# Performance work log

Hardware: AMD Instinct MI355X
Metric: run time of the kernel (lower is better)

The kernel has to match this reference:

```python
import jax, jax.numpy as jnp
import numpy as np

B, N, HID, HEADS = 4, 512, 64, 4
D = HID // HEADS          # head_dim = 16
E_DIM = 1
SCALE = 1.0 / np.sqrt(D)
LN_EPS = 1e-5
NEG = -1e9


def _linear_init(k, fan_in, fan_out):
    lim = 1.0 / np.sqrt(fan_in)
    kw, kb = jax.random.split(k)
    W = jax.random.uniform(kw, (fan_in, fan_out), jnp.float32, -lim, lim)
    b = jax.random.uniform(kb, (fan_out,), jnp.float32, -lim, lim)
    return W, b


def setup_inputs() -> dict:
    key = jax.random.key(0)
    ks = jax.random.split(key, 8)
    W1_w, W1_b = _linear_init(ks[3], HID, HID)
    W2_w, W2_b = _linear_init(ks[4], HID, HID)
    W3_w, W3_b = _linear_init(ks[5], HID, HID)
    W4_w, W4_b = _linear_init(ks[6], HID, HID)
    W5_w, W5_b = _linear_init(ks[7], E_DIM, HID)
    return {
        "x": jax.random.normal(ks[0], (B, N, HID), jnp.float32),
        "adj": jax.random.randint(ks[1], (B, N, N), 0, 2, jnp.int32),
        "edge_features": jax.random.normal(ks[2], (B, N, N, E_DIM), jnp.float32),
        "W1_w": W1_w, "W1_b": W1_b,
        "W2_w": W2_w, "W2_b": W2_b,
        "W3_w": W3_w, "W3_b": W3_b,
        "W4_w": W4_w, "W4_b": W4_b,
        "W5_w": W5_w, "W5_b": W5_b,
        "ln_g": jnp.ones((HID,), jnp.float32),
        "ln_b": jnp.zeros((HID,), jnp.float32),
    }


def _layer_norm(y, g, b):
    m = jnp.mean(y, axis=-1, keepdims=True)
    v = jnp.mean(jnp.square(y - m), axis=-1, keepdims=True)
    return (y - m) * jax.lax.rsqrt(v + LN_EPS) * g + b


def reference(x, adj, edge_features, W1_w, W1_b, W2_w, W2_b, W3_w, W3_b,
              W4_w, W4_b, W5_w, W5_b, ln_g, ln_b):
    b, n, h = x.shape
    self_t = x @ W1_w + W1_b                               # [B,N,HID]
    Q = (x @ W3_w + W3_b).reshape(b, n, HEADS, D)          # [B,N,H,D]
    K = (x @ W4_w + W4_b).reshape(b, n, HEADS, D)          # [B,N,H,D]
    # edge contribution: W5 e_ij -> [B,N,N,H,D] (the big intermediate)
    Ec = (edge_features @ W5_w + W5_b).reshape(b, n, n, HEADS, D)
    # (Q_i . (K_j + E_ij)) split into node-pair GEMM + edge broadcast term
    scores = (jnp.einsum('bihd,bjhd->bhij', Q, K)
              + jnp.einsum('bihd,bijhd->bhij', Q, Ec)) * SCALE  # [B,H,N,N]
    scores = jnp.where(adj[:, None, :, :] == 0, NEG, scores)
    attn = jax.nn.softmax(scores, axis=-1)                 # dropout = identity (eval)
    V = (x @ W2_w + W2_b).reshape(b, n, HEADS, D)          # [B,N,H,D]
    msg = jnp.einsum('bhij,bjhd->bihd', attn, V).reshape(b, n, h)
    return _layer_norm(x + self_t + msg, ln_g, ln_b)
```

## Files before the change

### kernel.cpp

```cpp
#include <hip/hip_runtime.h>

#define B 4
#define N 512
#define HID 64
#define HEADS 4
#define DH 16
#define SCALE 0.25f
#define NEG (-1e9f)
#define LN_EPS 1e-5f

constexpr int ROWS = B * N;
constexpr size_t OFF_ST  = 0;
constexpr size_t OFF_Q   = (size_t)ROWS * HID;
constexpr size_t OFF_K   = 2 * OFF_Q;
constexpr size_t OFF_V   = 3 * OFF_Q;
constexpr size_t OFF_MSG = 4 * OFF_Q;

__global__ __launch_bounds__(256) void proj_kernel(
    const float* __restrict__ x,
    const float* __restrict__ W1w, const float* __restrict__ W1b,
    const float* __restrict__ W2w, const float* __restrict__ W2b,
    const float* __restrict__ W3w, const float* __restrict__ W3b,
    const float* __restrict__ W4w, const float* __restrict__ W4b,
    float* __restrict__ ws)
{
  __shared__ float xsT[64 * 8];
  const int t = threadIdx.x;
  const int rows0 = blockIdx.x * 8;

  if (t < 128) {
    const float4 v = *(const float4*)&x[(size_t)rows0 * HID + t * 4];
    const int r = t >> 4;
    const int k0 = (t & 15) * 4;
    xsT[(k0 + 0) * 8 + r] = v.x;
    xsT[(k0 + 1) * 8 + r] = v.y;
    xsT[(k0 + 2) * 8 + r] = v.z;
    xsT[(k0 + 3) * 8 + r] = v.w;
  }
  __syncthreads();

  const int m = t >> 6;
  const int c = t & 63;
  const float* Ww; const float* Wb; size_t off;
  if      (m == 0) { Ww = W1w; Wb = W1b; off = OFF_ST; }
  else if (m == 1) { Ww = W3w; Wb = W3b; off = OFF_Q;  }
  else if (m == 2) { Ww = W4w; Wb = W4b; off = OFF_K;  }
  else             { Ww = W2w; Wb = W2b; off = OFF_V;  }

  float acc[8];
#pragma unroll
  for (int r = 0; r < 8; ++r) acc[r] = 0.f;

#pragma unroll 16
  for (int k = 0; k < 64; ++k) {
    const float w = Ww[(k << 6) + c];
    const float* xr = &xsT[k * 8];
    const float4 a0 = *(const float4*)(xr);
    const float4 a1 = *(const float4*)(xr + 4);
    acc[0] = fmaf(a0.x, w, acc[0]); acc[1] = fmaf(a0.y, w, acc[1]);
    acc[2] = fmaf(a0.z, w, acc[2]); acc[3] = fmaf(a0.w, w, acc[3]);
    acc[4] = fmaf(a1.x, w, acc[4]); acc[5] = fmaf(a1.y, w, acc[5]);
    acc[6] = fmaf(a1.z, w, acc[6]); acc[7] = fmaf(a1.w, w, acc[7]);
  }

  const float bias = Wb[c];
  const size_t base = off + (size_t)rows0 * HID + c;
#pragma unroll
  for (int r = 0; r < 8; ++r)
    ws[base + (size_t)r * HID] = acc[r] + bias;
}

__global__ __launch_bounds__(256, 2) void attn_kernel(
    const int*   __restrict__ adj,
    const float* __restrict__ efeat,
    const float* __restrict__ W5w, const float* __restrict__ W5b,
    float* __restrict__ ws)
{
  __shared__ float Ksh[N * 20];
  __shared__ float Vsh[N * 20];

  const int it = blockIdx.x, h = blockIdx.y, b = blockIdx.z;
  const int t = threadIdx.x;
  const int g  = t & 15;
  const int il = t >> 4;
  const int i  = it * 16 + il;

  const float* Qb = ws + OFF_Q;
  const float* Kb = ws + OFF_K;
  const float* Vb = ws + OFF_V;
  float* msg = ws + OFF_MSG;

  {
    const int jj = t >> 2;
    const int dq = (t & 3) << 2;
#pragma unroll
    for (int p = 0; p < 8; ++p) {
      const int j = jj + (p << 6);
      const size_t gb = ((size_t)(b * N + j)) * HID + h * DH + dq;
      *(float4*)&Ksh[j * 20 + dq] = *(const float4*)&Kb[gb];
      *(float4*)&Vsh[j * 20 + dq] = *(const float4*)&Vb[gb];
    }
  }

  const float* qrow = Qb + ((size_t)(b * N + i)) * HID + h * DH;
  const float4 q0 = *(const float4*)(qrow);
  const float4 q1 = *(const float4*)(qrow + 4);
  const float4 q2 = *(const float4*)(qrow + 8);
  const float4 q3 = *(const float4*)(qrow + 12);
  const float4 w50 = *(const float4*)&W5w[h * DH];
  const float4 w51 = *(const float4*)&W5w[h * DH + 4];
  const float4 w52 = *(const float4*)&W5w[h * DH + 8];
  const float4 w53 = *(const float4*)&W5w[h * DH + 12];
  const float4 b50 = *(const float4*)&W5b[h * DH];
  const float4 b51 = *(const float4*)&W5b[h * DH + 4];
  const float4 b52 = *(const float4*)&W5b[h * DH + 8];
  const float4 b53 = *(const float4*)&W5b[h * DH + 12];
  const float qw5 = q0.x*w50.x + q0.y*w50.y + q0.z*w50.z + q0.w*w50.w
                  + q1.x*w51.x + q1.y*w51.y + q1.z*w51.z + q1.w*w51.w
                  + q2.x*w52.x + q2.y*w52.y + q2.z*w52.z + q2.w*w52.w
                  + q3.x*w53.x + q3.y*w53.y + q3.z*w53.z + q3.w*w53.w;
  const float qb5 = q0.x*b50.x + q0.y*b50.y + q0.z*b50.z + q0.w*b50.w
                  + q1.x*b51.x + q1.y*b51.y + q1.z*b51.z + q1.w*b51.w
                  + q2.x*b52.x + q2.y*b52.y + q2.z*b52.z + q2.w*b52.w
                  + q3.x*b53.x + q3.y*b53.y + q3.z*b53.z + q3.w*b53.w;

  __syncthreads();

  const int*   adjRow = adj   + ((size_t)(b * N + i)) * N;
  const float* eRow   = efeat + ((size_t)(b * N + i)) * N;

  float s[32];
#pragma unroll
  for (int jj = 0; jj < 32; ++jj) {
    const int j = g + (jj << 4);
    const int   a  = adjRow[j];
    const float ev = eRow[j];
    const float* kr = &Ksh[j * 20];
    const float4 k0 = *(const float4*)(kr);
    const float4 k1 = *(const float4*)(kr + 4);
    const float4 k2 = *(const float4*)(kr + 8);
    const float4 k3 = *(const float4*)(kr + 12);
    float sA = q0.x*k0.x, sB = q0.y*k0.y, sC = q0.z*k0.z, sD = q0.w*k0.w;
    sA = fmaf(q1.x,k1.x,sA); sB = fmaf(q1.y,k1.y,sB);
    sC = fmaf(q1.z,k1.z,sC); sD = fmaf(q1.w,k1.w,sD);
    sA = fmaf(q2.x,k2.x,sA); sB = fmaf(q2.y,k2.y,sB);
    sC = fmaf(q2.z,k2.z,sC); sD = fmaf(q2.w,k2.w,sD);
    sA = fmaf(q3.x,k3.x,sA); sB = fmaf(q3.y,k3.y,sB);
    sC = fmaf(q3.z,k3.z,sC); sD = fmaf(q3.w,k3.w,sD);
    const float sc = ((sA + sB) + (sC + sD) + ev * qw5 + qb5) * SCALE;
    s[jj] = (a == 0) ? NEG : sc;
  }

  float r16[16], r8[8], r4[4];
#pragma unroll
  for (int k = 0; k < 16; ++k) r16[k] = fmaxf(s[k], s[k + 16]);
#pragma unroll
  for (int k = 0; k < 8;  ++k) r8[k]  = fmaxf(r16[k], r16[k + 8]);
#pragma unroll
  for (int k = 0; k < 4;  ++k) r4[k]  = fmaxf(r8[k], r8[k + 4]);
  float M = fmaxf(fmaxf(r4[0], r4[1]), fmaxf(r4[2], r4[3]));
#pragma unroll
  for (int o = 1; o < 16; o <<= 1) M = fmaxf(M, __shfl_xor(M, o, 16));

  float l0 = 0.f, l1 = 0.f, l2 = 0.f, l3 = 0.f;
  float acc[16];
#pragma unroll
  for (int d = 0; d < 16; ++d) acc[d] = 0.f;

#pragma unroll
  for (int jj = 0; jj < 32; ++jj) {
    const int j = g + (jj << 4);
    const float p = __expf(s[jj] - M);
    if      ((jj & 3) == 0) l0 += p;
    else if ((jj & 3) == 1) l1 += p;
    else if ((jj & 3) == 2) l2 += p;
    else                    l3 += p;
    const float* vr = &Vsh[j * 20];
    const float4 v0 = *(const float4*)(vr);
    const float4 v1 = *(const float4*)(vr + 4);
    const float4 v2 = *(const float4*)(vr + 8);
    const float4 v3 = *(const float4*)(vr + 12);
    acc[0]  = fmaf(p, v0.x, acc[0]);  acc[1]  = fmaf(p, v0.y, acc[1]);
    acc[2]  = fmaf(p, v0.z, acc[2]);  acc[3]  = fmaf(p, v0.w, acc[3]);
    acc[4]  = fmaf(p, v1.x, acc[4]);  acc[5]  = fmaf(p, v1.y, acc[5]);
    acc[6]  = fmaf(p, v1.z, acc[6]);  acc[7]  = fmaf(p, v1.w, acc[7]);
    acc[8]  = fmaf(p, v2.x, acc[8]);  acc[9]  = fmaf(p, v2.y, acc[9]);
    acc[10] = fmaf(p, v2.z, acc[10]); acc[11] = fmaf(p, v2.w, acc[11]);
    acc[12] = fmaf(p, v3.x, acc[12]); acc[13] = fmaf(p, v3.y, acc[13]);
    acc[14] = fmaf(p, v3.z, acc[14]); acc[15] = fmaf(p, v3.w, acc[15]);
  }

  float lw = (l0 + l1) + (l2 + l3);
#pragma unroll
  for (int o = 1; o < 16; o <<= 1) lw += __shfl_xor(lw, o, 16);

  __syncthreads();
  float* P = Ksh;
  const int prow = (il * 16 + g) * 20;
  *(float4*)&P[prow +  0] = make_float4(acc[0],  acc[1],  acc[2],  acc[3]);
  *(float4*)&P[prow +  4] = make_float4(acc[4],  acc[5],  acc[6],  acc[7]);
  *(float4*)&P[prow +  8] = make_float4(acc[8],  acc[9],  acc[10], acc[11]);
  *(float4*)&P[prow + 12] = make_float4(acc[12], acc[13], acc[14], acc[15]);
  __syncthreads();

  float ssum = 0.f;
#pragma unroll
  for (int gp = 0; gp < 16; ++gp)
    ssum += P[(il * 16 + gp) * 20 + g];

  msg[((size_t)(b * N + i)) * HID + h * DH + g] = ssum * (1.0f / lw);
}

__global__ __launch_bounds__(256) void ln_kernel(
    const float* __restrict__ x, const float* __restrict__ ws,
    const float* __restrict__ gamma, const float* __restrict__ beta,
    float* __restrict__ out)
{
  const int t = threadIdx.x;
  const int lane = t & 63;
  const int row = blockIdx.x * 4 + (t >> 6);
  const size_t idx = (size_t)row * HID + lane;
  const float* ST  = ws + OFF_ST;
  const float* MSG = ws + OFF_MSG;

  const float v = x[idx] + ST[idx] + MSG[idx];
  float mu = v;
#pragma unroll
  for (int o = 1; o < 64; o <<= 1) mu += __shfl_xor(mu, o, 64);
  mu *= (1.0f / 64.0f);
  const float dv = v - mu;
  float var = dv * dv;
#pragma unroll
  for (int o = 1; o < 64; o <<= 1) var += __shfl_xor(var, o, 64);
  var *= (1.0f / 64.0f);
  out[idx] = dv * rsqrtf(var + LN_EPS) * gamma[lane] + beta[lane];
}

extern "C" void kernel_launch(void* const* d_in, const int* in_sizes, int n_in,
                              void* d_out, int out_size, void* d_ws, size_t ws_size,
                              hipStream_t stream)
{
  const float* x   = (const float*)d_in[0];
  const int*   adj = (const int*)d_in[1];
  const float* ef  = (const float*)d_in[2];
  const float* W1w = (const float*)d_in[3];
  const float* W1b = (const float*)d_in[4];
  const float* W2w = (const float*)d_in[5];
  const float* W2b = (const float*)d_in[6];
  const float* W3w = (const float*)d_in[7];
  const float* W3b = (const float*)d_in[8];
  const float* W4w = (const float*)d_in[9];
  const float* W4b = (const float*)d_in[10];
  const float* W5w = (const float*)d_in[11];
  const float* W5b = (const float*)d_in[12];
  const float* lng = (const float*)d_in[13];
  const float* lnb = (const float*)d_in[14];
  float* ws  = (float*)d_ws;
  float* out = (float*)d_out;

  proj_kernel<<<ROWS / 8, 256, 0, stream>>>(x, W1w, W1b, W2w, W2b, W3w, W3b, W4w, W4b, ws);
  attn_kernel<<<dim3(32, HEADS, B), 256, 0, stream>>>(adj, ef, W5w, W5b, ws);
  ln_kernel<<<ROWS / 4, 256, 0, stream>>>(x, ws, lng, lnb, out);
}
```

Before: 24.00 us.

## Fuse layernorm into attention kernel via last-block atomic counter

Removes the separate layernorm launch. Each attention block atomically bumps a per-(batch, row-tile) counter after storing its head's message slice. The fourth-arriving block then applies the residual sum and layernorm for those 16 rows. The counters are zeroed in the projection kernel, and release/acquire fences order the cross-block message visibility. This saves a kernel launch and its tail, at the cost of atomics, an extra barrier, and imbalance where one block of the four does the extra work.

```diff
diff --git a/kernel.cpp b/kernel.cpp
--- a/kernel.cpp
+++ b/kernel.cpp
@@ -15,6 +15,7 @@
 constexpr size_t OFF_K   = 2 * OFF_Q;
 constexpr size_t OFF_V   = 3 * OFF_Q;
 constexpr size_t OFF_MSG = 4 * OFF_Q;
+constexpr size_t OFF_CNT = 5 * OFF_Q;
 
 __global__ __launch_bounds__(256) void proj_kernel(
     const float* __restrict__ x,
@@ -28,6 +29,9 @@
   const int t = threadIdx.x;
   const int rows0 = blockIdx.x * 8;
 
+  if (blockIdx.x == 0 && t < 128)
+    ((int*)(ws + OFF_CNT))[t] = 0;
+
   if (t < 128) {
     const float4 v = *(const float4*)&x[(size_t)rows0 * HID + t * 4];
     const int r = t >> 4;
@@ -74,7 +78,9 @@
     const int*   __restrict__ adj,
     const float* __restrict__ efeat,
     const float* __restrict__ W5w, const float* __restrict__ W5b,
-    float* __restrict__ ws)
+    const float* __restrict__ x,
+    const float* __restrict__ lng, const float* __restrict__ lnb,
+    float* __restrict__ ws, float* __restrict__ out)
 {
   __shared__ float Ksh[N * 20];
   __shared__ float Vsh[N * 20];
@@ -208,32 +214,46 @@
   for (int gp = 0; gp < 16; ++gp)
     ssum += P[(il * 16 + gp) * 20 + g];
 
-  msg[((size_t)(b * N + i)) * HID + h * DH + g] = ssum * (1.0f / lw);
-}
-
-__global__ __launch_bounds__(256) void ln_kernel(
-    const float* __restrict__ x, const float* __restrict__ ws,
-    const float* __restrict__ gamma, const float* __restrict__ beta,
-    float* __restrict__ out)
-{
-  const int t = threadIdx.x;
-  const int lane = t & 63;
-  const int row = blockIdx.x * 4 + (t >> 6);
-  const size_t idx = (size_t)row * HID + lane;
-  const float* ST  = ws + OFF_ST;
-  const float* MSG = ws + OFF_MSG;
-
-  const float v = x[idx] + ST[idx] + MSG[idx];
-  float mu = v;
-#pragma unroll
-  for (int o = 1; o < 64; o <<= 1) mu += __shfl_xor(mu, o, 64);
-  mu *= (1.0f / 64.0f);
-  const float dv = v - mu;
-  float var = dv * dv;
-#pragma unroll
-  for (int o = 1; o < 64; o <<= 1) var += __shfl_xor(var, o, 64);
-  var *= (1.0f / 64.0f);
-  out[idx] = dv * rsqrtf(var + LN_EPS) * gamma[lane] + beta[lane];
+  const float msgv = ssum * (1.0f / lw);
+  __hip_atomic_store(&msg[((size_t)(b * N + i)) * HID + h * DH + g], msgv,
+                     __ATOMIC_RELAXED, __HIP_MEMORY_SCOPE_AGENT);
+
+  volatile int* lastFlag = (volatile int*)&Ksh[8192];
+  __syncthreads();
+  if (t == 0) {
+    __builtin_amdgcn_fence(__ATOMIC_RELEASE, "agent");
+    int* cnt = (int*)(ws + OFF_CNT) + (b * 32 + it);
+    const int old = __hip_atomic_fetch_add(cnt, 1, __ATOMIC_ACQ_REL,
+                                           __HIP_MEMORY_SCOPE_AGENT);
+    *lastFlag = (old == 3) ? 1 : 0;
+  }
+  __syncthreads();
+  if (*lastFlag == 0) return;
+  __builtin_amdgcn_fence(__ATOMIC_ACQUIRE, "agent");
+
+  {
+    const int col = t & 63;
+    const int wv  = t >> 6;
+    const float* ST = ws + OFF_ST;
+#pragma unroll
+    for (int k = 0; k < 4; ++k) {
+      const int lr = wv + 4 * k;
+      const size_t gi = (size_t)(b * N + it * 16 + lr) * HID + col;
+      const float mg = __hip_atomic_load(&msg[gi], __ATOMIC_RELAXED,
+                                         __HIP_MEMORY_SCOPE_AGENT);
+      const float v = x[gi] + ST[gi] + mg;
+      float mu = v;
+#pragma unroll
+      for (int o = 1; o < 64; o <<= 1) mu += __shfl_xor(mu, o, 64);
+      mu *= (1.0f / 64.0f);
+      const float dv = v - mu;
+      float var = dv * dv;
+#pragma unroll
+      for (int o = 1; o < 64; o <<= 1) var += __shfl_xor(var, o, 64);
+      var *= (1.0f / 64.0f);
+      out[gi] = dv * rsqrtf(var + LN_EPS) * lng[col] + lnb[col];
+    }
+  }
 }
 
 extern "C" void kernel_launch(void* const* d_in, const int* in_sizes, int n_in,
@@ -259,6 +279,5 @@
   float* out = (float*)d_out;
 
   proj_kernel<<<ROWS / 8, 256, 0, stream>>>(x, W1w, W1b, W2w, W2b, W3w, W3b, W4w, W4b, ws);
-  attn_kernel<<<dim3(32, HEADS, B), 256, 0, stream>>>(adj, ef, W5w, W5b, ws);
-  ln_kernel<<<ROWS / 4, 256, 0, stream>>>(x, ws, lng, lnb, out);
+  attn_kernel<<<dim3(32, HEADS, B), 256, 0, stream>>>(adj, ef, W5w, W5b, x, lng, lnb, ws, out);
 }
```

Result: slower. 35.64 us (+48.5%).

## Split attention over key halves and merge partial softmax in layer-norm kernel

Applied to the files above, without the earlier changes.

Splits the key dimension of the attention kernel into two halves, doubling the grid to 1024 blocks and halving shared memory per block so more blocks fit per CU. Each block writes unnormalized partial accumulators plus its running max and sum, and the layer-norm kernel combines the two halves with a flash-decoding style rescale. This targets low occupancy and the small grid (512 blocks on a 256-CU device), at the cost of duplicated K/V staging and Q setup plus extra partial-record traffic and exps in the final kernel.

```diff
diff --git a/kernel.cpp b/kernel.cpp
--- a/kernel.cpp
+++ b/kernel.cpp
@@ -14,7 +14,7 @@
 constexpr size_t OFF_Q   = (size_t)ROWS * HID;
 constexpr size_t OFF_K   = 2 * OFF_Q;
 constexpr size_t OFF_V   = 3 * OFF_Q;
-constexpr size_t OFF_MSG = 4 * OFF_Q;
+constexpr size_t OFF_PART= 4 * OFF_Q;
 
 __global__ __launch_bounds__(256) void proj_kernel(
     const float* __restrict__ x,
@@ -70,16 +70,19 @@
     ws[base + (size_t)r * HID] = acc[r] + bias;
 }
 
-__global__ __launch_bounds__(256, 2) void attn_kernel(
+__global__ __launch_bounds__(256, 4) void attn_kernel(
     const int*   __restrict__ adj,
     const float* __restrict__ efeat,
     const float* __restrict__ W5w, const float* __restrict__ W5b,
     float* __restrict__ ws)
 {
-  __shared__ float Ksh[N * 20];
-  __shared__ float Vsh[N * 20];
-
-  const int it = blockIdx.x, h = blockIdx.y, b = blockIdx.z;
+  __shared__ float Ksh[256 * 20];
+  __shared__ float Vsh[256 * 20];
+
+  const int it = blockIdx.x, h = blockIdx.y;
+  const int b    = blockIdx.z >> 1;
+  const int half = blockIdx.z & 1;
+  const int j0   = half << 8;
   const int t = threadIdx.x;
   const int g  = t & 15;
   const int il = t >> 4;
@@ -88,15 +91,15 @@
   const float* Qb = ws + OFF_Q;
   const float* Kb = ws + OFF_K;
   const float* Vb = ws + OFF_V;
-  float* msg = ws + OFF_MSG;
+  float* part = ws + OFF_PART;
 
   {
-    const int jj = t >> 2;
+    const int sj = t >> 2;
     const int dq = (t & 3) << 2;
 #pragma unroll
-    for (int p = 0; p < 8; ++p) {
-      const int j = jj + (p << 6);
-      const size_t gb = ((size_t)(b * N + j)) * HID + h * DH + dq;
+    for (int p = 0; p < 4; ++p) {
+      const int j = sj + (p << 6);
+      const size_t gb = ((size_t)(b * N + j0 + j)) * HID + h * DH + dq;
       *(float4*)&Ksh[j * 20 + dq] = *(const float4*)&Kb[gb];
       *(float4*)&Vsh[j * 20 + dq] = *(const float4*)&Vb[gb];
     }
@@ -126,12 +129,12 @@
 
   __syncthreads();
 
-  const int*   adjRow = adj   + ((size_t)(b * N + i)) * N;
-  const float* eRow   = efeat + ((size_t)(b * N + i)) * N;
-
-  float s[32];
-#pragma unroll
-  for (int jj = 0; jj < 32; ++jj) {
+  const int*   adjRow = adj   + ((size_t)(b * N + i)) * N + j0;
+  const float* eRow   = efeat + ((size_t)(b * N + i)) * N + j0;
+
+  float s[16];
+#pragma unroll
+  for (int jj = 0; jj < 16; ++jj) {
     const int j = g + (jj << 4);
     const int   a  = adjRow[j];
     const float ev = eRow[j];
@@ -151,30 +154,25 @@
     s[jj] = (a == 0) ? NEG : sc;
   }
 
-  float r16[16], r8[8], r4[4];
-#pragma unroll
-  for (int k = 0; k < 16; ++k) r16[k] = fmaxf(s[k], s[k + 16]);
-#pragma unroll
-  for (int k = 0; k < 8;  ++k) r8[k]  = fmaxf(r16[k], r16[k + 8]);
-#pragma unroll
-  for (int k = 0; k < 4;  ++k) r4[k]  = fmaxf(r8[k], r8[k + 4]);
+  float r8[8], r4[4];
+#pragma unroll
+  for (int k = 0; k < 8; ++k) r8[k] = fmaxf(s[k], s[k + 8]);
+#pragma unroll
+  for (int k = 0; k < 4; ++k) r4[k] = fmaxf(r8[k], r8[k + 4]);
   float M = fmaxf(fmaxf(r4[0], r4[1]), fmaxf(r4[2], r4[3]));
 #pragma unroll
   for (int o = 1; o < 16; o <<= 1) M = fmaxf(M, __shfl_xor(M, o, 16));
 
-  float l0 = 0.f, l1 = 0.f, l2 = 0.f, l3 = 0.f;
+  float l0 = 0.f, l1 = 0.f;
   float acc[16];
 #pragma unroll
   for (int d = 0; d < 16; ++d) acc[d] = 0.f;
 
 #pragma unroll
-  for (int jj = 0; jj < 32; ++jj) {
+  for (int jj = 0; jj < 16; ++jj) {
     const int j = g + (jj << 4);
     const float p = __expf(s[jj] - M);
-    if      ((jj & 3) == 0) l0 += p;
-    else if ((jj & 3) == 1) l1 += p;
-    else if ((jj & 3) == 2) l2 += p;
-    else                    l3 += p;
+    if (jj & 1) l1 += p; else l0 += p;
     const float* vr = &Vsh[j * 20];
     const float4 v0 = *(const float4*)(vr);
     const float4 v1 = *(const float4*)(vr + 4);
@@ -190,7 +188,7 @@
     acc[14] = fmaf(p, v3.z, acc[14]); acc[15] = fmaf(p, v3.w, acc[15]);
   }
 
-  float lw = (l0 + l1) + (l2 + l3);
+  float lw = l0 + l1;
 #pragma unroll
   for (int o = 1; o < 16; o <<= 1) lw += __shfl_xor(lw, o, 16);
 
@@ -208,7 +206,9 @@
   for (int gp = 0; gp < 16; ++gp)
     ssum += P[(il * 16 + gp) * 20 + g];
 
-  msg[((size_t)(b * N + i)) * HID + h * DH + g] = ssum * (1.0f / lw);
+  float* rec = part + ((((size_t)(b * N + i)) * HEADS + h) * 2 + half) * 18;
+  rec[g] = ssum;
+  if (g == 0) { rec[16] = M; rec[17] = lw; }
 }
 
 __global__ __launch_bounds__(256) void ln_kernel(
@@ -220,10 +220,20 @@
   const int lane = t & 63;
   const int row = blockIdx.x * 4 + (t >> 6);
   const size_t idx = (size_t)row * HID + lane;
-  const float* ST  = ws + OFF_ST;
-  const float* MSG = ws + OFF_MSG;
-
-  const float v = x[idx] + ST[idx] + MSG[idx];
+  const float* ST   = ws + OFF_ST;
+  const float* part = ws + OFF_PART;
+
+  const int h = lane >> 4;
+  const int d = lane & 15;
+  const float* rec0 = part + (((size_t)row * HEADS + h) * 2 + 0) * 18;
+  const float* rec1 = rec0 + 18;
+  const float a0 = rec0[d], m0 = rec0[16], e0 = rec0[17];
+  const float a1 = rec1[d], m1 = rec1[16], e1 = rec1[17];
+  const float M  = fmaxf(m0, m1);
+  const float w0 = __expf(m0 - M), w1 = __expf(m1 - M);
+  const float msg = (a0 * w0 + a1 * w1) / (e0 * w0 + e1 * w1);
+
+  const float v = x[idx] + ST[idx] + msg;
   float mu = v;
 #pragma unroll
   for (int o = 1; o < 64; o <<= 1) mu += __shfl_xor(mu, o, 64);
@@ -259,6 +269,6 @@
   float* out = (float*)d_out;
 
   proj_kernel<<<ROWS / 8, 256, 0, stream>>>(x, W1w, W1b, W2w, W2b, W3w, W3b, W4w, W4b, ws);
-  attn_kernel<<<dim3(32, HEADS, B), 256, 0, stream>>>(adj, ef, W5w, W5b, ws);
+  attn_kernel<<<dim3(32, HEADS, B * 2), 256, 0, stream>>>(adj, ef, W5w, W5b, ws);
   ln_kernel<<<ROWS / 4, 256, 0, stream>>>(x, ws, lng, lnb, out);
 }
```

Result: faster. 23.16 us (-3.5%).
